# Performance work log

Measured on AMD Instinct MI355X. Metric: run time of the kernel, lower is better.

## Reference

```python
import jax, jax.numpy as jnp
import numpy as np

N, F_IN, H, OUT, E = 50000, 128, 128, 40, 800000


def setup_inputs() -> dict:
    key = jax.random.key(0)
    ks = jax.random.split(key, 20)
    s = 0.05
    return {
        "x": jax.random.normal(ks[0], (N, F_IN), jnp.float32),
        "edge_index": jax.random.randint(ks[1], (2, E), 0, N, jnp.int64),
        # GATConv (heads=1)
        "W_gat": jax.random.normal(ks[2], (F_IN, H), jnp.float32) * s,
        "att_src": jax.random.normal(ks[3], (H,), jnp.float32) * s,
        "att_dst": jax.random.normal(ks[4], (H,), jnp.float32) * s,
        "b_gat": jnp.zeros((H,), jnp.float32),
        # GCNConv
        "W_gcn": jax.random.normal(ks[5], (F_IN, H), jnp.float32) * s,
        "b_gcn": jnp.zeros((H,), jnp.float32),
        # SAGEConv (mean aggr): lin_l on neighbors (with bias), lin_r on root (no bias)
        "W_sage_l": jax.random.normal(ks[6], (F_IN, H), jnp.float32) * s,
        "b_sage_l": jnp.zeros((H,), jnp.float32),
        "W_sage_r": jax.random.normal(ks[7], (F_IN, H), jnp.float32) * s,
        # MLP head
        "W1": jax.random.normal(ks[8], (3 * H, 2 * H), jnp.float32) * s,
        "b1": jnp.zeros((2 * H,), jnp.float32),
        "W2": jax.random.normal(ks[9], (2 * H, H), jnp.float32) * s,
        "b2": jnp.zeros((H,), jnp.float32),
        "W3": jax.random.normal(ks[10], (H, OUT), jnp.float32) * s,
        "b3": jnp.zeros((OUT,), jnp.float32),
        # BatchNorm1d(3H)
        "gamma": jnp.ones((3 * H,), jnp.float32),
        "beta": jnp.zeros((3 * H,), jnp.float32),
    }


def _add_self_loops(edge_index, n):
    loop = jnp.arange(n, dtype=edge_index.dtype)
    src = jnp.concatenate([edge_index[0], loop])
    dst = jnp.concatenate([edge_index[1], loop])
    return src, dst


def _gat(x, src, dst, n, W, att_src, att_dst, bias):
    h = x @ W                                   # [N, H]
    a_s = h @ att_src                           # [N]
    a_d = h @ att_dst                           # [N]
    e = jax.nn.leaky_relu(a_s[src] + a_d[dst], 0.2)  # [E']
    m = jax.ops.segment_max(e, dst, num_segments=n)
    ex = jnp.exp(e - m[dst])
    denom = jax.ops.segment_sum(ex, dst, num_segments=n)
    alpha = ex / denom[dst]
    out = jax.ops.segment_sum(alpha[:, None] * h[src], dst, num_segments=n)
    return out + bias


def _gcn(x, src, dst, n, W, bias):
    h = x @ W
    deg = jax.ops.segment_sum(jnp.ones_like(dst, dtype=h.dtype), dst, num_segments=n)
    dinv = jnp.where(deg > 0, jax.lax.rsqrt(deg), 0.0)
    norm = dinv[src] * dinv[dst]                # [E']
    out = jax.ops.segment_sum(norm[:, None] * h[src], dst, num_segments=n)
    return out + bias


def _sage(x, src, dst, n, W_l, b_l, W_r):
    agg = jax.ops.segment_sum(x[src], dst, num_segments=n)
    cnt = jax.ops.segment_sum(jnp.ones_like(dst, dtype=x.dtype), dst, num_segments=n)
    mean = agg / jnp.maximum(cnt, 1.0)[:, None]
    return mean @ W_l + b_l + x @ W_r


def reference(x, edge_index, W_gat, att_src, att_dst, b_gat, W_gcn, b_gcn,
              W_sage_l, b_sage_l, W_sage_r, W1, b1, W2, b2, W3, b3, gamma, beta):
    n = x.shape[0]
    src, dst = edge_index[0], edge_index[1]          # SAGE: no self-loops
    src_sl, dst_sl = _add_self_loops(edge_index, n)  # GAT/GCN add self-loops

    x_gat = _gat(x, src_sl, dst_sl, n, W_gat, att_src, att_dst, b_gat)
    x_gcn = _gcn(x, src_sl, dst_sl, n, W_gcn, b_gcn)
    x_sage = _sage(x, src, dst, n, W_sage_l, b_sage_l, W_sage_r)

    h = jnp.concatenate([x_gat, x_gcn, x_sage], axis=1)  # [N, 3H]
    # BatchNorm1d (training-mode batch statistics; biased variance, eps=1e-5)
    mu = h.mean(axis=0)
    var = h.var(axis=0)
    h = (h - mu) * jax.lax.rsqrt(var + 1e-5) * gamma + beta
    # dropout is identity at inference
    h = jax.nn.relu(h) @ W1 + b1
    h = jax.nn.relu(h) @ W2 + b2
    h = jax.nn.relu(h) @ W3 + b3
    return h
```

## Files before the change

### kernel.cpp

```cpp
#include <hip/hip_runtime.h>
#include <cstdint>
#include <cstddef>

#define NN   50000
#define FIN  128
#define HD   128
#define EE   800000
#define C3   384
#define NOUT 40

#define NBLK ((NN + 127) / 128)

#define SPLIT_BLKS ((NN + 4) / 4)

#define NBUCK ((NN + 511) / 512)
#define BCAP  16384
#define BK_BLKS ((EE + 8191) / 8192)
#define SCAP  12288

#define RCAP      136
#define STORE_CAP 128
#define ZROW NN

#define LDSW 132

typedef __attribute__((ext_vector_type(8))) short s8v;
typedef __attribute__((ext_vector_type(4))) float f4v;
typedef __attribute__((ext_vector_type(8))) ushort u8v;

typedef const __attribute__((address_space(1))) unsigned int* guintp;
typedef __attribute__((address_space(3))) unsigned int* luintp;

static __device__ __forceinline__ void async_copy16(const void* g, void* l) {
    __builtin_amdgcn_global_load_lds((guintp)g, (luintp)l, 16, 0, 0);
}

static __device__ __forceinline__ float b2f(ushort u) {
    return __uint_as_float((unsigned)u << 16);
}
static __device__ __forceinline__ ushort f2b(float v) {
    unsigned u = __float_as_uint(v);
    unsigned r = u + 0x7fffu + ((u >> 16) & 1u);
    return (ushort)(r >> 16);
}

__global__ __launch_bounds__(256) void k_split_x_att(
    const float* __restrict__ x,
    const float* __restrict__ w_as, const float* __restrict__ w_ad,
    ushort* __restrict__ xb,
    float* __restrict__ a_s, float* __restrict__ a_d)
{
    int node = blockIdx.x * 4 + (threadIdx.x >> 6);
    if (node > NN) return;
    int lane = threadIdx.x & 63;
    size_t o = (size_t)node * 128 + lane * 2;
    if (node == NN) {
        ushort2 z; z.x = 0; z.y = 0;
        *(ushort2*)(xb + o) = z;
        return;
    }
    float2 v  = *(const float2*)(x + o);
    { ushort2 u; u.x = f2b(v.x); u.y = f2b(v.y); *(ushort2*)(xb + o) = u; }
    float2 w1 = *(const float2*)(w_as + lane * 2);
    float2 w2 = *(const float2*)(w_ad + lane * 2);
    float s1 = v.x * w1.x + v.y * w1.y;
    float s2 = v.x * w2.x + v.y * w2.y;
    #pragma unroll
    for (int off = 32; off; off >>= 1) {
        s1 += __shfl_down(s1, off);
        s2 += __shfl_down(s2, off);
    }
    if (lane == 0) { a_s[node] = s1; a_d[node] = s2; }
}

__global__ void k_splitw_all(
    const float* __restrict__ Wg, const float* __restrict__ Wc,
    const float* __restrict__ Wl, const float* __restrict__ Wr,
    const float* __restrict__ W1, const float* __restrict__ W2,
    const float* __restrict__ W3,
    const float* __restrict__ asv, const float* __restrict__ adv,
    float* __restrict__ w_as, float* __restrict__ w_ad,
    ushort* __restrict__ btg, ushort* __restrict__ btc,
    ushort* __restrict__ btsg,
    ushort* __restrict__ bt1, ushort* __restrict__ bt2,
    ushort* __restrict__ bt3)
{
    int ry = blockIdx.x;
    int t = threadIdx.x;
    if (ry == 816) {
        if (t < 128) {
            float s1 = 0.f, s2 = 0.f;
            for (int j = 0; j < 128; ++j) {
                float w = Wg[t * 128 + j];
                s1 += w * asv[j];
                s2 += w * adv[j];
            }
            w_as[t] = s1; w_ad[t] = s2;
        }
        return;
    }
    const float* W = nullptr; ushort* dh; int K, Nw, n;
    bool sage = false;
    if (ry < 128)      { n = ry;       K = 128; Nw = 128; W = Wg; dh = btg; }
    else if (ry < 256) { n = ry - 128; K = 128; Nw = 128; W = Wc; dh = btc; }
    else if (ry < 384) { n = ry - 256; K = 256; Nw = 128; sage = true; dh = btsg; }
    else if (ry < 640) { n = ry - 384; K = 384; Nw = 256; W = W1; dh = bt1; }
    else if (ry < 768) { n = ry - 640; K = 256; Nw = 128; W = W2; dh = bt2; }
    else               { n = ry - 768; K = 128; Nw = 40;  W = W3; dh = bt3; }
    for (int k = t; k < K; k += 256) {
        float v;
        if (sage) v = (k < 128) ? Wl[(size_t)k * 128 + n] : Wr[(size_t)(k - 128) * 128 + n];
        else      v = (n < Nw) ? W[(size_t)k * Nw + n] : 0.f;
        dh[(size_t)n * K + k] = f2b(v);
    }
}

template<int NT, int NCH, int AX, int BN>
__global__ __launch_bounds__(256, BN ? 4 : 5) void k_gemm2(
    const ushort* __restrict__ A, int K,
    const ushort* __restrict__ Bt,
    int M, int mode,
    const float* __restrict__ bias,
    float* __restrict__ Cf, int ldc,
    ushort* __restrict__ Ch, int ldch,
    int colmax,
    const float* __restrict__ bnscale, const float* __restrict__ bnshift)
{
    constexpr int COLS = NT * 16;
    constexpr int HOPU = 8 * COLS;
    constexpr int KTOT = NCH * 128;

    __shared__ __align__(16) ushort S[16384];
    __shared__ float bns[BN ? 768 : 4];
    ushort* Bs = S;
    ushort* As = S + 8192;

    const int lane = threadIdx.x & 63;
    const int wave = threadIdx.x >> 6;
    const int quad = lane >> 4;
    const int ln15 = lane & 15;
    const int brow = AX ? blockIdx.y : blockIdx.x;
    const int bcol = AX ? blockIdx.x : blockIdx.y;
    const int row0 = brow * 128 + wave * 32;
    const int col0 = bcol * COLS;
    const int Rbase = brow * 128;

    auto stageB = [&](int c, int h) {
        for (int u0 = wave * 64; u0 < HOPU; u0 += 256) {
            int u  = u0 + lane;
            int kq  = u / COLS;
            int col = u - kq * COLS;
            int kk  = c * 128 + h * 64 + kq * 8;
            const ushort* gp = Bt + (size_t)(col0 + col) * KTOT + kk;
            async_copy16(gp, (char*)Bs + (size_t)u0 * 16);
        }
    };
    auto stageA = [&](int c, int h) {
        #pragma unroll
        for (int i = 0; i < 4; ++i) {
            int u0 = (wave * 4 + i) * 64;
            int u  = u0 + lane;
            int row = u >> 3;
            int s   = u & 7;
            int sg  = s ^ (row & 7);
            int rr = Rbase + row; if (rr > M - 1) rr = M - 1;
            int kk = c * 128 + h * 64 + sg * 8;
            const ushort* gp = A + (size_t)rr * K + kk;
            async_copy16(gp, (char*)As + (size_t)u0 * 16);
        }
    };
    auto afrag = [&](int jj, int mt) -> s8v {
        int r = wave * 32 + mt * 16 + ln15;
        int sg = jj * 4 + quad;
        int unit = r * 8 + (sg ^ (r & 7));
        return *(const s8v*)(As + (size_t)unit * 8);
    };

    f4v acc[2][NT] = {};

    auto compute = [&](int jj, int kk0) {
        s8v a0 = afrag(jj, 0);
        s8v a1 = afrag(jj, 1);
        if constexpr (BN) {
            int cb0 = kk0 + (jj * 4 + quad) * 8;
            #pragma unroll
            for (int e = 0; e < 8; ++e) {
                float sc = bns[cb0 + e];
                float sh = bns[384 + cb0 + e];
                float v0 = b2f((ushort)a0[e]) * sc + sh;
                float v1 = b2f((ushort)a1[e]) * sc + sh;
                v0 = v0 > 0.f ? v0 : 0.f;
                v1 = v1 > 0.f ? v1 : 0.f;
                a0[e] = (short)f2b(v0);
                a1[e] = (short)f2b(v1);
            }
        }
        #pragma unroll
        for (int t = 0; t < NT; ++t) {
            int ub = (jj * 4 + quad) * COLS + t * 16 + ln15;
            s8v b = *(const s8v*)(Bs + (size_t)ub * 8);
            acc[0][t] = __builtin_amdgcn_mfma_f32_16x16x32_bf16(a0, b, acc[0][t], 0, 0, 0);
            acc[1][t] = __builtin_amdgcn_mfma_f32_16x16x32_bf16(a1, b, acc[1][t], 0, 0, 0);
        }
    };

    if constexpr (BN) {
        for (int j = threadIdx.x; j < 384; j += 256) {
            bns[j] = bnscale[j];
            bns[384 + j] = bnshift[j];
        }
    }
    stageB(0, 0); stageA(0, 0);
    __syncthreads();

    #pragma unroll
    for (int ph = 0; ph < NCH; ++ph) {
        #pragma unroll
        for (int h = 0; h < 2; ++h) {
            int kk0 = ph * 128 + h * 64;
            compute(0, kk0); compute(1, kk0);
            if (!(ph == NCH - 1 && h == 1)) {
                __syncthreads();
                int nc = ph, nh = h + 1;
                if (nh == 2) { nh = 0; ++nc; }
                stageB(nc, nh); stageA(nc, nh);
                __syncthreads();
            }
        }
    }

    if (NT == 8 && mode == 0) {
        __syncthreads();
        ushort* Lp = S + wave * 2176;
        #pragma unroll
        for (int mt = 0; mt < 2; ++mt) {
            #pragma unroll
            for (int t = 0; t < NT; ++t) {
                int cc = col0 + t * 16 + ln15;
                #pragma unroll
                for (int r = 0; r < 4; ++r) {
                    float v = acc[mt][t][r] + bias[cc];
                    v = v > 0.f ? v : 0.f;
                    Lp[(quad * 4 + r) * LDSW + t * 16 + ln15] = f2b(v);
                }
            }
            int cb = (lane & 31) * 4;
            #pragma unroll
            for (int it = 0; it < 8; ++it) {
                int row2 = it * 2 + (lane >> 5);
                int rr = row0 + mt * 16 + row2;
                uint2 v = *(uint2*)(Lp + row2 * LDSW + cb);
                if (rr < M)
                    *(uint2*)(Ch + (size_t)rr * ldch + col0 + cb) = v;
            }
        }
    } else {
        #pragma unroll
        for (int t = 0; t < NT; ++t) {
            int cc = col0 + t * 16 + ln15;
            #pragma unroll
            for (int mt = 0; mt < 2; ++mt) {
                #pragma unroll
                for (int r = 0; r < 4; ++r) {
                    int rr = row0 + mt * 16 + quad * 4 + r;
                    if (rr < M && cc < colmax)
                        Cf[(size_t)rr * ldc + cc] = acc[mt][t][r] + bias[cc];
                }
            }
        }
    }
}

__global__ __launch_bounds__(256, 3) void k_gemm_prod(
    const ushort* __restrict__ tgb, const ushort* __restrict__ tcb,
    const ushort* __restrict__ tsb, const ushort* __restrict__ xb,
    const ushort* __restrict__ btg, const ushort* __restrict__ btc,
    const ushort* __restrict__ btsg,
    const float* __restrict__ bg, const float* __restrict__ bc,
    const float* __restrict__ bsl,
    float* __restrict__ pS, float* __restrict__ pQ,
    ushort* __restrict__ hch)
{
    constexpr int COLS = 128;
    constexpr int HOPU = 8 * COLS;
    __shared__ __align__(16) ushort S[16384];
    ushort* Bs = S;
    ushort* As = S + 8192;
    float* red = (float*)(S + 14336);

    const int z = blockIdx.z;
    const ushort* A1 = (z == 0) ? tgb : (z == 1) ? tcb : tsb;
    const ushort* Bt = (z == 0) ? btg : (z == 1) ? btc : btsg;
    const float*  bias = (z == 0) ? bg : (z == 1) ? bc : bsl;
    const int nch = (z == 2) ? 2 : 1;
    const int ktot = nch * 128;

    const int lane = threadIdx.x & 63;
    const int wave = threadIdx.x >> 6;
    const int quad = lane >> 4;
    const int ln15 = lane & 15;
    const int row0 = blockIdx.x * 128 + wave * 32;
    const int Rbase = blockIdx.x * 128;

    auto stageB = [&](int c, int h) {
        for (int u0 = wave * 64; u0 < HOPU; u0 += 256) {
            int u  = u0 + lane;
            int kq  = u / COLS;
            int col = u - kq * COLS;
            int kk  = c * 128 + h * 64 + kq * 8;
            const ushort* gp = Bt + (size_t)col * ktot + kk;
            async_copy16(gp, (char*)Bs + (size_t)u0 * 16);
        }
    };
    auto stageA = [&](int c, int h) {
        #pragma unroll
        for (int i = 0; i < 4; ++i) {
            int u0 = (wave * 4 + i) * 64;
            int u  = u0 + lane;
            int row = u >> 3;
            int s   = u & 7;
            int sg  = s ^ (row & 7);
            int rr = Rbase + row; if (rr > NN - 1) rr = NN - 1;
            int kk = c * 128 + h * 64 + sg * 8;
            const ushort* gp = (kk < 128) ? (A1 + (size_t)rr * 128 + kk)
                                          : (xb + (size_t)rr * 128 + (kk - 128));
            async_copy16(gp, (char*)As + (size_t)u0 * 16);
        }
    };
    auto afrag = [&](int jj, int mt) -> s8v {
        int r = wave * 32 + mt * 16 + ln15;
        int sg = jj * 4 + quad;
        int unit = r * 8 + (sg ^ (r & 7));
        return *(const s8v*)(As + (size_t)unit * 8);
    };

    f4v acc[2][8] = {};

    auto compute = [&](int jj) {
        s8v a0 = afrag(jj, 0);
        s8v a1 = afrag(jj, 1);
        #pragma unroll
        for (int t = 0; t < 8; ++t) {
            int ub = (jj * 4 + quad) * COLS + t * 16 + ln15;
            s8v b = *(const s8v*)(Bs + (size_t)ub * 8);
            acc[0][t] = __builtin_amdgcn_mfma_f32_16x16x32_bf16(a0, b, acc[0][t], 0, 0, 0);
            acc[1][t] = __builtin_amdgcn_mfma_f32_16x16x32_bf16(a1, b, acc[1][t], 0, 0, 0);
        }
    };

    stageB(0, 0); stageA(0, 0);
    __syncthreads();

    for (int ph = 0; ph < nch; ++ph) {
        for (int h = 0; h < 2; ++h) {
            compute(0); compute(1);
            if (!(ph == nch - 1 && h == 1)) {
                __syncthreads();
                int nc = ph, nh = h + 1;
                if (nh == 2) { nh = 0; ++nc; }
                stageB(nc, nh); stageA(nc, nh);
                __syncthreads();
            }
        }
    }

    __syncthreads();
    if (threadIdx.x < 256) red[threadIdx.x] = 0.f;
    ushort* Lp = S + wave * 2176;
    float sp[8] = {}, qp[8] = {};
    #pragma unroll
    for (int mt = 0; mt < 2; ++mt) {
        #pragma unroll
        for (int t = 0; t < 8; ++t) {
            #pragma unroll
            for (int r = 0; r < 4; ++r) {
                int rr = row0 + mt * 16 + quad * 4 + r;
                float v = acc[mt][t][r] + bias[t * 16 + ln15];
                Lp[(quad * 4 + r) * LDSW + t * 16 + ln15] = f2b(v);
                if (rr < NN) { sp[t] += v; qp[t] += v * v; }
            }
        }
        int cb = (lane & 31) * 4;
        #pragma unroll
        for (int it = 0; it < 8; ++it) {
            int row2 = it * 2 + (lane >> 5);
            int rr = row0 + mt * 16 + row2;
            uint2 v = *(uint2*)(Lp + row2 * LDSW + cb);
            if (rr < NN)
                *(uint2*)(hch + (size_t)rr * C3 + z * 128 + cb) = v;
        }
    }
    __syncthreads();
    #pragma unroll
    for (int t = 0; t < 8; ++t) {
        float s = sp[t], q = qp[t];
        s += __shfl_xor(s, 16); s += __shfl_xor(s, 32);
        q += __shfl_xor(q, 16); q += __shfl_xor(q, 32);
        if (quad == 0) {
            atomicAdd(&red[t * 16 + ln15], s);
            atomicAdd(&red[128 + t * 16 + ln15], q);
        }
    }
    __syncthreads();
    if (threadIdx.x < 128) {
        size_t o = (size_t)blockIdx.x * C3 + z * 128 + threadIdx.x;
        pS[o] = red[threadIdx.x];
        pQ[o] = red[128 + threadIdx.x];
    }
}

__global__ __launch_bounds__(1024) void k_bucket(
    const int* __restrict__ e_src, const int* __restrict__ e_dst,
    int* __restrict__ bcnt, uint* __restrict__ ebuf)
{
    __shared__ uint sval[8192];
    __shared__ int scnt[NBUCK], sbase[NBUCK];
    int t = threadIdx.x;
    if (t < NBUCK) scnt[t] = 0;
    __syncthreads();
    int e0 = blockIdx.x * 8192;
    #pragma unroll
    for (int i = 0; i < 8; ++i) {
        int g = e0 + i * 1024 + t;
        uint val = 0xffffffffu;
        if (g < EE) {
            int d = e_dst[g];
            int s = e_src[g];
            int b = d >> 9;
            val = ((uint)b << 25) | ((uint)(d & 511) << 16) | (uint)s;
            atomicAdd(&scnt[b], 1);
        }
        sval[i * 1024 + t] = val;
    }
    __syncthreads();
    if (t < NBUCK) {
        sbase[t] = atomicAdd(&bcnt[t], scnt[t]);
        scnt[t] = 0;
    }
    __syncthreads();
    #pragma unroll
    for (int i = 0; i < 8; ++i) {
        uint val = sval[i * 1024 + t];
        if (val != 0xffffffffu) {
            int b = val >> 25;
            int lo = atomicAdd(&scnt[b], 1);
            ebuf[(size_t)b * BCAP + sbase[b] + lo] = val;
        }
    }
}

__global__ __launch_bounds__(1024) void k_degscan(
    const int* __restrict__ bcnt, const uint* __restrict__ ebuf,
    int* __restrict__ offs, float* __restrict__ dinv)
{
    __shared__ int hist[512];
    __shared__ int sh[256];
    __shared__ int btop;
    int b = blockIdx.x, t = threadIdx.x;
    int d0 = b * 512;
    if (t < 512) hist[t] = 0;
    __syncthreads();
    int nb = bcnt[b];
    const uint* eb = ebuf + (size_t)b * BCAP;
    for (int i = t; i < nb; i += 1024)
        atomicAdd(&hist[(eb[i] >> 16) & 511], 1);
    __syncthreads();
    if (t < 64) {
        int acc = 0;
        for (int i = t; i < b; i += 64) {
            int nd = NN - i * 512; if (nd > 512) nd = 512;
            acc += bcnt[i] + nd;
        }
        #pragma unroll
        for (int off = 32; off; off >>= 1) acc += __shfl_down(acc, off);
        if (t == 0) btop = acc;
    }
    int v0 = 0, v1 = 0;
    if (t < 256) {
        int i0g = d0 + t * 2;
        v0 = (i0g < NN) ? hist[t * 2] + 1 : 0;
        v1 = (i0g + 1 < NN) ? hist[t * 2 + 1] + 1 : 0;
        sh[t] = v0 + v1;
    }
    __syncthreads();
    for (int off = 1; off < 256; off <<= 1) {
        int u = 0;
        if (t < 256 && t >= off) u = sh[t - off];
        __syncthreads();
        if (t < 256) sh[t] += u;
        __syncthreads();
    }
    if (t < 256) {
        int pair = v0 + v1;
        int excl = sh[t] - pair + btop;
        int i0g = d0 + t * 2;
        if (i0g < NN)     { offs[i0g] = excl;          dinv[i0g] = rsqrtf((float)v0); }
        if (i0g + 1 < NN) { offs[i0g + 1] = excl + v0; dinv[i0g + 1] = rsqrtf((float)v1); }
        if (b == NBUCK - 1 && t == 255) offs[NN] = excl + pair;
    }
}

__global__ __launch_bounds__(1024) void k_csr_build(
    const int* __restrict__ bcnt, const uint* __restrict__ ebuf,
    const int* __restrict__ offs, ushort* __restrict__ esrc)
{
    __shared__ ushort sout[SCAP];
    __shared__ int cur[512];
    int b = blockIdx.x, t = threadIdx.x;
    int d0 = b * 512;
    int ndst = NN - d0; if (ndst > 512) ndst = 512;
    int obase = offs[d0];
    if (t < ndst) cur[t] = offs[d0 + t] - obase;
    __syncthreads();
    int nb = bcnt[b];
    const uint* eb = ebuf + (size_t)b * BCAP;
    for (int i = t; i < nb; i += 1024) {
        uint val = eb[i];
        int slot = atomicAdd(&cur[(val >> 16) & 511], 1);
        sout[slot] = (ushort)(val & 0xffffu);
    }
    if (t < ndst) {
        int slot = atomicAdd(&cur[t], 1);
        sout[slot] = (ushort)(d0 + t);
    }
    __syncthreads();
    int total = offs[d0 + ndst] - obase;
    for (int i = t; i < total; i += 1024)
        esrc[obase + i] = sout[i];
}

__global__ __launch_bounds__(256, 6) void k_gather(
    const ushort* __restrict__ esrc, const int* __restrict__ offs,
    const float* __restrict__ a_s, const float* __restrict__ a_d,
    const float* __restrict__ dinv,
    const ushort* __restrict__ xb,
    ushort* __restrict__ tgb, ushort* __restrict__ tcb,
    ushort* __restrict__ tsb)
{
    __shared__ uint2 recs[16][RCAP];
    int t = threadIdx.x;
    int qid = t >> 4;
    int ln = t & 15;
    int d = blockIdx.x * 16 + qid;
    if (d >= NN) return;
    uint2* rec = recs[qid];
    int beg = offs[d], end = offs[d + 1];
    int cnt = end - beg;
    float ad = a_d[d], dd = dinv[d];
    int stored = cnt < STORE_CAP ? cnt : STORE_CAP;

    float mloc = -3.0e38f;
    for (int b = 0; b < cnt; b += 16) {
        int j = b + ln;
        if (j < cnt) {
            int s = esrc[beg + j];
            float e = a_s[s] + ad;
            e = (e > 0.f) ? e : 0.2f * e;
            mloc = fmaxf(mloc, e);
            if (j < STORE_CAP) {
                uint2 r;
                r.x = __float_as_uint(e);
                r.y = (uint)s | ((uint)f2b(dinv[s] * dd) << 16);
                rec[j] = r;
            }
        }
    }
    float m = mloc;
    #pragma unroll
    for (int off = 1; off < 16; off <<= 1) m = fmaxf(m, __shfl_xor(m, off, 16));

    float denl = 0.f;
    for (int j = ln; j < stored; j += 16) {
        float ex = expf(__uint_as_float(rec[j].x) - m);
        denl += ex;
        rec[j].x = __float_as_uint(ex);
    }
    for (int idx = beg + STORE_CAP + ln; idx < end; idx += 16) {
        int s = esrc[idx];
        float e = a_s[s] + ad;
        e = (e > 0.f) ? e : 0.2f * e;
        denl += expf(e - m);
    }
    float den = denl;
    #pragma unroll
    for (int off = 1; off < 16; off <<= 1) den += __shfl_xor(den, off, 16);
    float rden = 1.f / den;

    for (int j = ln; j < stored; j += 16) {
        uint2 r = rec[j];
        uint2 q;
        q.x = (uint)f2b(__uint_as_float(r.x) * rden) | (r.y & 0xffff0000u);
        q.y = r.y & 0xffffu;
        rec[j] = q;
    }
    if (ln < 8) { uint2 q; q.x = 0u; q.y = (uint)ZROW; rec[stored + ln] = q; }

    float tg[8] = {}, tc[8] = {}, ts[8] = {};
    const ushort* xbs = xb + ln * 8;
    auto ldx = [&](uint srow) -> u8v {
        return *(const u8v*)(xbs + (size_t)srow * 128);
    };
    auto fmacc = [&](u8v x8, uint pw) {
        float wg = __uint_as_float(pw << 16);
        float wc = __uint_as_float(pw & 0xffff0000u);
        #pragma unroll
        for (int k = 0; k < 8; ++k) {
            float xv = b2f(x8[k]);
            tg[k] += wg * xv;
            tc[k] += wc * xv;
            ts[k] += xv;
        }
    };

    int P4 = (stored + 3) & ~3;
    uint pa0, pa1, pa2, pa3, pb0, pb1, pb2, pb3;
    u8v xa0, xa1, xa2, xa3, ya0, ya1, ya2, ya3;
    {
        uint2 r0 = rec[0], r1 = rec[1], r2 = rec[2], r3 = rec[3];
        pa0 = r0.x; xa0 = ldx(r0.y);
        pa1 = r1.x; xa1 = ldx(r1.y);
        pa2 = r2.x; xa2 = ldx(r2.y);
        pa3 = r3.x; xa3 = ldx(r3.y);
    }
    int j = 0;
    for (;;) {
        { uint2 r0 = rec[j+4], r1 = rec[j+5], r2 = rec[j+6], r3 = rec[j+7];
          pb0 = r0.x; ya0 = ldx(r0.y);
          pb1 = r1.x; ya1 = ldx(r1.y);
          pb2 = r2.x; ya2 = ldx(r2.y);
          pb3 = r3.x; ya3 = ldx(r3.y); }
        fmacc(xa0, pa0); fmacc(xa1, pa1); fmacc(xa2, pa2); fmacc(xa3, pa3);
        j += 4; if (j >= P4) break;
        { uint2 r0 = rec[j+4], r1 = rec[j+5], r2 = rec[j+6], r3 = rec[j+7];
          pa0 = r0.x; xa0 = ldx(r0.y);
          pa1 = r1.x; xa1 = ldx(r1.y);
          pa2 = r2.x; xa2 = ldx(r2.y);
          pa3 = r3.x; xa3 = ldx(r3.y); }
        fmacc(ya0, pb0); fmacc(ya1, pb1); fmacc(ya2, pb2); fmacc(ya3, pb3);
        j += 4; if (j >= P4) break;
    }

    for (int base = beg + STORE_CAP; base < end; base += 16) {
        int idx = base + ln;
        int s = ZROW; uint pw = 0;
        if (idx < end) {
            int ss = esrc[idx];
            float e = a_s[ss] + ad;
            e = (e > 0.f) ? e : 0.2f * e;
            pw = (uint)f2b(expf(e - m) * rden) | ((uint)f2b(dinv[ss] * dd) << 16);
            s = ss;
        }
        int cb = end - base; if (cb > 16) cb = 16;
        for (int jj = 0; jj < cb; ++jj) {
            int sa = __shfl(s, jj, 16);
            uint pa = (uint)__shfl((int)pw, jj, 16);
            fmacc(ldx((uint)sa), pa);
        }
    }

    u8v xd = *(const u8v*)(xb + (size_t)d * 128 + ln * 8);
    int cs = cnt - 1;
    float rc = 1.f / (float)(cs > 1 ? cs : 1);
    u8v og, oc, os;
    #pragma unroll
    for (int k = 0; k < 8; ++k) {
        og[k] = f2b(tg[k]);
        oc[k] = f2b(tc[k]);
        os[k] = f2b((ts[k] - b2f(xd[k])) * rc);
    }
    size_t row = (size_t)d * 128 + ln * 8;
    *(u8v*)(tgb + row) = og;
    *(u8v*)(tcb + row) = oc;
    *(u8v*)(tsb + row) = os;
}

__global__ void k_bn_final(const float* __restrict__ pS, const float* __restrict__ pQ,
                           const float* __restrict__ gamma, const float* __restrict__ beta,
                           float* __restrict__ scale, float* __restrict__ shift)
{
    int j = blockIdx.x * 64 + threadIdx.x;
    if (j >= C3) return;
    float s = 0.f, q = 0.f;
    for (int r = 0; r < NBLK; ++r) {
        s += pS[(size_t)r * C3 + j];
        q += pQ[(size_t)r * C3 + j];
    }
    const float rn = 1.f / (float)NN;
    float mu  = s * rn;
    float var = q * rn - mu * mu;
    float sc  = gamma[j] * rsqrtf(var + 1e-5f);
    scale[j] = sc;
    shift[j] = beta[j] - mu * sc;
}

extern "C" void kernel_launch(void* const* d_in, const int* in_sizes, int n_in,
                              void* d_out, int out_size, void* d_ws, size_t ws_size,
                              hipStream_t stream) {
    const float* x        = (const float*)d_in[0];
    const int*   ei       = (const int*)d_in[1];
    const float* W_gat    = (const float*)d_in[2];
    const float* att_src  = (const float*)d_in[3];
    const float* att_dst  = (const float*)d_in[4];
    const float* b_gat    = (const float*)d_in[5];
    const float* W_gcn    = (const float*)d_in[6];
    const float* b_gcn    = (const float*)d_in[7];
    const float* W_sage_l = (const float*)d_in[8];
    const float* b_sage_l = (const float*)d_in[9];
    const float* W_sage_r = (const float*)d_in[10];
    const float* W1       = (const float*)d_in[11];
    const float* b1       = (const float*)d_in[12];
    const float* W2       = (const float*)d_in[13];
    const float* b2       = (const float*)d_in[14];
    const float* W3       = (const float*)d_in[15];
    const float* b3       = (const float*)d_in[16];
    const float* gamma    = (const float*)d_in[17];
    const float* beta     = (const float*)d_in[18];

    const int* e_src = ei;
    const int* e_dst = ei + EE;

    char* base = (char*)d_ws;
    size_t o = 0;
    ushort* hch  = (ushort*)(base + o); o += (size_t)NN * C3 * 2;
    ushort* tgb  = (ushort*)(base + o); o += (size_t)NN * 128 * 2;
    ushort* tcb  = (ushort*)(base + o); o += (size_t)NN * 128 * 2;
    ushort* tsb  = (ushort*)(base + o); o += (size_t)NN * 128 * 2;
    ushort* xb   = (ushort*)(base + o); o += (size_t)(NN + 1) * 128 * 2;
    ushort* esrc = (ushort*)(base + o); o += ((size_t)(EE + NN) * 2 + 15) & ~15ull;
    int*    offs = (int*)(base + o);    o += (size_t)(NN + 16) * 4;
    float*  as_  = (float*)(base + o);  o += (size_t)NN * 4;
    float*  ad_  = (float*)(base + o);  o += (size_t)NN * 4;
    float*  dinv = (float*)(base + o);  o += (size_t)NN * 4;
    int*    bcnt = (int*)(base + o);    o += 128 * 4;
    float*  pS   = (float*)(base + o);  o += (size_t)NBLK * C3 * 4;
    float*  pQ   = (float*)(base + o);  o += (size_t)NBLK * C3 * 4;
    float*  scale= (float*)(base + o);  o += C3 * 4;
    float*  shift= (float*)(base + o);  o += C3 * 4;
    float*  w_as = (float*)(base + o);  o += 128 * 4;
    float*  w_ad = (float*)(base + o);  o += 128 * 4;
    ushort* btg  = (ushort*)(base + o); o += 128 * 128 * 2;
    ushort* btc  = (ushort*)(base + o); o += 128 * 128 * 2;
    ushort* btsg = (ushort*)(base + o); o += 128 * 256 * 2;
    ushort* bt1  = (ushort*)(base + o); o += 256 * 384 * 2;
    ushort* bt2  = (ushort*)(base + o); o += 128 * 256 * 2;
    ushort* bt3  = (ushort*)(base + o); o += 48 * 128 * 2;
    ushort* a1 = tgb;
    ushort* a2 = tsb;
    uint*   ebuf = (uint*)hch;

    hipMemsetAsync(bcnt, 0, 128 * 4, stream);

    k_splitw_all<<<817, 256, 0, stream>>>(W_gat, W_gcn, W_sage_l, W_sage_r, W1, W2, W3,
        att_src, att_dst, w_as, w_ad, btg, btc, btsg, bt1, bt2, bt3);
    k_split_x_att<<<SPLIT_BLKS, 256, 0, stream>>>(x, w_as, w_ad, xb, as_, ad_);

    k_bucket<<<BK_BLKS, 1024, 0, stream>>>(e_src, e_dst, bcnt, ebuf);
    k_degscan<<<NBUCK, 1024, 0, stream>>>(bcnt, ebuf, offs, dinv);
    k_csr_build<<<NBUCK, 1024, 0, stream>>>(bcnt, ebuf, offs, esrc);

    k_gather<<<(NN + 15) / 16, 256, 0, stream>>>(
        esrc, offs, as_, ad_, dinv, xb, tgb, tcb, tsb);

    k_gemm_prod<<<dim3(NBLK, 1, 3), 256, 0, stream>>>(
        tgb, tcb, tsb, xb, btg, btc, btsg,
        b_gat, b_gcn, b_sage_l, pS, pQ, hch);

    k_bn_final<<<6, 64, 0, stream>>>(pS, pQ, gamma, beta, scale, shift);

    k_gemm2<8, 3, 1, 1><<<dim3(2, NBLK), 256, 0, stream>>>(
        hch, 384, bt1, NN, 0, b1, nullptr, 0, a1, 256, 256, scale, shift);
    k_gemm2<8, 2, 0, 0><<<dim3(NBLK, 1), 256, 0, stream>>>(
        a1, 256, bt2, NN, 0, b2, nullptr, 0, a2, 128, 128, nullptr, nullptr);
    k_gemm2<3, 1, 0, 0><<<dim3(NBLK, 1), 256, 0, stream>>>(
        a2, 128, bt3, NN, 2, b3, (float*)d_out, NOUT, nullptr, 0, NOUT, nullptr, nullptr);
}
```

Baseline: 310.2 us.

## Fuse launch chain: merge bucket/weight prep, CSR build/x split, and final two GEMMs

Merges the weight-prep kernel into the edge bucketing launch and the x-to-bf16/attention-score kernel into a combined degree-scan plus CSR build kernel, which cuts the launch count. The last two MLP GEMMs are fused into one kernel that keeps the intermediate 128-wide activation in LDS and runs the 40-column output GEMM from there, so the a2 round trip through global memory goes away. The fused GEMM uses more LDS and has a lower occupancy bound. The k_bn_final block size changes and RCAP is reduced.

```diff
diff --git a/kernel.cpp b/kernel.cpp
--- a/kernel.cpp
+++ b/kernel.cpp
@@ -11,18 +11,18 @@
 
 #define NBLK ((NN + 127) / 128)
 
-#define SPLIT_BLKS ((NN + 4) / 4)
-
 #define NBUCK ((NN + 511) / 512)
 #define BCAP  16384
 #define BK_BLKS ((EE + 8191) / 8192)
 #define SCAP  12288
-
-#define RCAP      136
+#define SXB   ((NN + 16) / 16)
+
+#define RCAP      132
 #define STORE_CAP 128
 #define ZROW NN
 
 #define LDSW 132
+#define A2W  136
 
 typedef __attribute__((ext_vector_type(8))) short s8v;
 typedef __attribute__((ext_vector_type(4))) float f4v;
@@ -44,36 +44,9 @@
     return (ushort)(r >> 16);
 }
 
-__global__ __launch_bounds__(256) void k_split_x_att(
-    const float* __restrict__ x,
-    const float* __restrict__ w_as, const float* __restrict__ w_ad,
-    ushort* __restrict__ xb,
-    float* __restrict__ a_s, float* __restrict__ a_d)
-{
-    int node = blockIdx.x * 4 + (threadIdx.x >> 6);
-    if (node > NN) return;
-    int lane = threadIdx.x & 63;
-    size_t o = (size_t)node * 128 + lane * 2;
-    if (node == NN) {
-        ushort2 z; z.x = 0; z.y = 0;
-        *(ushort2*)(xb + o) = z;
-        return;
-    }
-    float2 v  = *(const float2*)(x + o);
-    { ushort2 u; u.x = f2b(v.x); u.y = f2b(v.y); *(ushort2*)(xb + o) = u; }
-    float2 w1 = *(const float2*)(w_as + lane * 2);
-    float2 w2 = *(const float2*)(w_ad + lane * 2);
-    float s1 = v.x * w1.x + v.y * w1.y;
-    float s2 = v.x * w2.x + v.y * w2.y;
-    #pragma unroll
-    for (int off = 32; off; off >>= 1) {
-        s1 += __shfl_down(s1, off);
-        s2 += __shfl_down(s2, off);
-    }
-    if (lane == 0) { a_s[node] = s1; a_d[node] = s2; }
-}
-
-__global__ void k_splitw_all(
+__global__ __launch_bounds__(1024) void k_bucketw(
+    const int* __restrict__ e_src, const int* __restrict__ e_dst,
+    int* __restrict__ bcnt, uint* __restrict__ ebuf,
     const float* __restrict__ Wg, const float* __restrict__ Wc,
     const float* __restrict__ Wl, const float* __restrict__ Wr,
     const float* __restrict__ W1, const float* __restrict__ W2,
@@ -85,337 +58,39 @@
     ushort* __restrict__ bt1, ushort* __restrict__ bt2,
     ushort* __restrict__ bt3)
 {
-    int ry = blockIdx.x;
     int t = threadIdx.x;
-    if (ry == 816) {
-        if (t < 128) {
-            float s1 = 0.f, s2 = 0.f;
-            for (int j = 0; j < 128; ++j) {
-                float w = Wg[t * 128 + j];
-                s1 += w * asv[j];
-                s2 += w * adv[j];
-            }
-            w_as[t] = s1; w_ad[t] = s2;
+    if (blockIdx.x >= BK_BLKS) {
+        int ry = blockIdx.x - BK_BLKS;
+        if (ry == 816) {
+            if (t < 128) {
+                float s1 = 0.f, s2 = 0.f;
+                for (int j = 0; j < 128; ++j) {
+                    float w = Wg[t * 128 + j];
+                    s1 += w * asv[j];
+                    s2 += w * adv[j];
+                }
+                w_as[t] = s1; w_ad[t] = s2;
+            }
+            return;
+        }
+        const float* W = nullptr; ushort* dh; int K, Nw, n;
+        bool sage = false;
+        if (ry < 128)      { n = ry;       K = 128; Nw = 128; W = Wg; dh = btg; }
+        else if (ry < 256) { n = ry - 128; K = 128; Nw = 128; W = Wc; dh = btc; }
+        else if (ry < 384) { n = ry - 256; K = 256; Nw = 128; sage = true; dh = btsg; }
+        else if (ry < 640) { n = ry - 384; K = 384; Nw = 256; W = W1; dh = bt1; }
+        else if (ry < 768) { n = ry - 640; K = 256; Nw = 128; W = W2; dh = bt2; }
+        else               { n = ry - 768; K = 128; Nw = 40;  W = W3; dh = bt3; }
+        for (int k = t; k < K; k += 1024) {
+            float v;
+            if (sage) v = (k < 128) ? Wl[(size_t)k * 128 + n] : Wr[(size_t)(k - 128) * 128 + n];
+            else      v = (n < Nw) ? W[(size_t)k * Nw + n] : 0.f;
+            dh[(size_t)n * K + k] = f2b(v);
         }
         return;
     }
-    const float* W = nullptr; ushort* dh; int K, Nw, n;
-    bool sage = false;
-    if (ry < 128)      { n = ry;       K = 128; Nw = 128; W = Wg; dh = btg; }
-    else if (ry < 256) { n = ry - 128; K = 128; Nw = 128; W = Wc; dh = btc; }
-    else if (ry < 384) { n = ry - 256; K = 256; Nw = 128; sage = true; dh = btsg; }
-    else if (ry < 640) { n = ry - 384; K = 384; Nw = 256; W = W1; dh = bt1; }
-    else if (ry < 768) { n = ry - 640; K = 256; Nw = 128; W = W2; dh = bt2; }
-    else               { n = ry - 768; K = 128; Nw = 40;  W = W3; dh = bt3; }
-    for (int k = t; k < K; k += 256) {
-        float v;
-        if (sage) v = (k < 128) ? Wl[(size_t)k * 128 + n] : Wr[(size_t)(k - 128) * 128 + n];
-        else      v = (n < Nw) ? W[(size_t)k * Nw + n] : 0.f;
-        dh[(size_t)n * K + k] = f2b(v);
-    }
-}
-
-template<int NT, int NCH, int AX, int BN>
-__global__ __launch_bounds__(256, BN ? 4 : 5) void k_gemm2(
-    const ushort* __restrict__ A, int K,
-    const ushort* __restrict__ Bt,
-    int M, int mode,
-    const float* __restrict__ bias,
-    float* __restrict__ Cf, int ldc,
-    ushort* __restrict__ Ch, int ldch,
-    int colmax,
-    const float* __restrict__ bnscale, const float* __restrict__ bnshift)
-{
-    constexpr int COLS = NT * 16;
-    constexpr int HOPU = 8 * COLS;
-    constexpr int KTOT = NCH * 128;
-
-    __shared__ __align__(16) ushort S[16384];
-    __shared__ float bns[BN ? 768 : 4];
-    ushort* Bs = S;
-    ushort* As = S + 8192;
-
-    const int lane = threadIdx.x & 63;
-    const int wave = threadIdx.x >> 6;
-    const int quad = lane >> 4;
-    const int ln15 = lane & 15;
-    const int brow = AX ? blockIdx.y : blockIdx.x;
-    const int bcol = AX ? blockIdx.x : blockIdx.y;
-    const int row0 = brow * 128 + wave * 32;
-    const int col0 = bcol * COLS;
-    const int Rbase = brow * 128;
-
-    auto stageB = [&](int c, int h) {
-        for (int u0 = wave * 64; u0 < HOPU; u0 += 256) {
-            int u  = u0 + lane;
-            int kq  = u / COLS;
-            int col = u - kq * COLS;
-            int kk  = c * 128 + h * 64 + kq * 8;
-            const ushort* gp = Bt + (size_t)(col0 + col) * KTOT + kk;
-            async_copy16(gp, (char*)Bs + (size_t)u0 * 16);
-        }
-    };
-    auto stageA = [&](int c, int h) {
-        #pragma unroll
-        for (int i = 0; i < 4; ++i) {
-            int u0 = (wave * 4 + i) * 64;
-            int u  = u0 + lane;
-            int row = u >> 3;
-            int s   = u & 7;
-            int sg  = s ^ (row & 7);
-            int rr = Rbase + row; if (rr > M - 1) rr = M - 1;
-            int kk = c * 128 + h * 64 + sg * 8;
-            const ushort* gp = A + (size_t)rr * K + kk;
-            async_copy16(gp, (char*)As + (size_t)u0 * 16);
-        }
-    };
-    auto afrag = [&](int jj, int mt) -> s8v {
-        int r = wave * 32 + mt * 16 + ln15;
-        int sg = jj * 4 + quad;
-        int unit = r * 8 + (sg ^ (r & 7));
-        return *(const s8v*)(As + (size_t)unit * 8);
-    };
-
-    f4v acc[2][NT] = {};
-
-    auto compute = [&](int jj, int kk0) {
-        s8v a0 = afrag(jj, 0);
-        s8v a1 = afrag(jj, 1);
-        if constexpr (BN) {
-            int cb0 = kk0 + (jj * 4 + quad) * 8;
-            #pragma unroll
-            for (int e = 0; e < 8; ++e) {
-                float sc = bns[cb0 + e];
-                float sh = bns[384 + cb0 + e];
-                float v0 = b2f((ushort)a0[e]) * sc + sh;
-                float v1 = b2f((ushort)a1[e]) * sc + sh;
-                v0 = v0 > 0.f ? v0 : 0.f;
-                v1 = v1 > 0.f ? v1 : 0.f;
-                a0[e] = (short)f2b(v0);
-                a1[e] = (short)f2b(v1);
-            }
-        }
-        #pragma unroll
-        for (int t = 0; t < NT; ++t) {
-            int ub = (jj * 4 + quad) * COLS + t * 16 + ln15;
-            s8v b = *(const s8v*)(Bs + (size_t)ub * 8);
-            acc[0][t] = __builtin_amdgcn_mfma_f32_16x16x32_bf16(a0, b, acc[0][t], 0, 0, 0);
-            acc[1][t] = __builtin_amdgcn_mfma_f32_16x16x32_bf16(a1, b, acc[1][t], 0, 0, 0);
-        }
-    };
-
-    if constexpr (BN) {
-        for (int j = threadIdx.x; j < 384; j += 256) {
-            bns[j] = bnscale[j];
-            bns[384 + j] = bnshift[j];
-        }
-    }
-    stageB(0, 0); stageA(0, 0);
-    __syncthreads();
-
-    #pragma unroll
-    for (int ph = 0; ph < NCH; ++ph) {
-        #pragma unroll
-        for (int h = 0; h < 2; ++h) {
-            int kk0 = ph * 128 + h * 64;
-            compute(0, kk0); compute(1, kk0);
-            if (!(ph == NCH - 1 && h == 1)) {
-                __syncthreads();
-                int nc = ph, nh = h + 1;
-                if (nh == 2) { nh = 0; ++nc; }
-                stageB(nc, nh); stageA(nc, nh);
-                __syncthreads();
-            }
-        }
-    }
-
-    if (NT == 8 && mode == 0) {
-        __syncthreads();
-        ushort* Lp = S + wave * 2176;
-        #pragma unroll
-        for (int mt = 0; mt < 2; ++mt) {
-            #pragma unroll
-            for (int t = 0; t < NT; ++t) {
-                int cc = col0 + t * 16 + ln15;
-                #pragma unroll
-                for (int r = 0; r < 4; ++r) {
-                    float v = acc[mt][t][r] + bias[cc];
-                    v = v > 0.f ? v : 0.f;
-                    Lp[(quad * 4 + r) * LDSW + t * 16 + ln15] = f2b(v);
-                }
-            }
-            int cb = (lane & 31) * 4;
-            #pragma unroll
-            for (int it = 0; it < 8; ++it) {
-                int row2 = it * 2 + (lane >> 5);
-                int rr = row0 + mt * 16 + row2;
-                uint2 v = *(uint2*)(Lp + row2 * LDSW + cb);
-                if (rr < M)
-                    *(uint2*)(Ch + (size_t)rr * ldch + col0 + cb) = v;
-            }
-        }
-    } else {
-        #pragma unroll
-        for (int t = 0; t < NT; ++t) {
-            int cc = col0 + t * 16 + ln15;
-            #pragma unroll
-            for (int mt = 0; mt < 2; ++mt) {
-                #pragma unroll
-                for (int r = 0; r < 4; ++r) {
-                    int rr = row0 + mt * 16 + quad * 4 + r;
-                    if (rr < M && cc < colmax)
-                        Cf[(size_t)rr * ldc + cc] = acc[mt][t][r] + bias[cc];
-                }
-            }
-        }
-    }
-}
-
-__global__ __launch_bounds__(256, 3) void k_gemm_prod(
-    const ushort* __restrict__ tgb, const ushort* __restrict__ tcb,
-    const ushort* __restrict__ tsb, const ushort* __restrict__ xb,
-    const ushort* __restrict__ btg, const ushort* __restrict__ btc,
-    const ushort* __restrict__ btsg,
-    const float* __restrict__ bg, const float* __restrict__ bc,
-    const float* __restrict__ bsl,
-    float* __restrict__ pS, float* __restrict__ pQ,
-    ushort* __restrict__ hch)
-{
-    constexpr int COLS = 128;
-    constexpr int HOPU = 8 * COLS;
-    __shared__ __align__(16) ushort S[16384];
-    ushort* Bs = S;
-    ushort* As = S + 8192;
-    float* red = (float*)(S + 14336);
-
-    const int z = blockIdx.z;
-    const ushort* A1 = (z == 0) ? tgb : (z == 1) ? tcb : tsb;
-    const ushort* Bt = (z == 0) ? btg : (z == 1) ? btc : btsg;
-    const float*  bias = (z == 0) ? bg : (z == 1) ? bc : bsl;
-    const int nch = (z == 2) ? 2 : 1;
-    const int ktot = nch * 128;
-
-    const int lane = threadIdx.x & 63;
-    const int wave = threadIdx.x >> 6;
-    const int quad = lane >> 4;
-    const int ln15 = lane & 15;
-    const int row0 = blockIdx.x * 128 + wave * 32;
-    const int Rbase = blockIdx.x * 128;
-
-    auto stageB = [&](int c, int h) {
-        for (int u0 = wave * 64; u0 < HOPU; u0 += 256) {
-            int u  = u0 + lane;
-            int kq  = u / COLS;
-            int col = u - kq * COLS;
-            int kk  = c * 128 + h * 64 + kq * 8;
-            const ushort* gp = Bt + (size_t)col * ktot + kk;
-            async_copy16(gp, (char*)Bs + (size_t)u0 * 16);
-        }
-    };
-    auto stageA = [&](int c, int h) {
-        #pragma unroll
-        for (int i = 0; i < 4; ++i) {
-            int u0 = (wave * 4 + i) * 64;
-            int u  = u0 + lane;
-            int row = u >> 3;
-            int s   = u & 7;
-            int sg  = s ^ (row & 7);
-            int rr = Rbase + row; if (rr > NN - 1) rr = NN - 1;
-            int kk = c * 128 + h * 64 + sg * 8;
-            const ushort* gp = (kk < 128) ? (A1 + (size_t)rr * 128 + kk)
-                                          : (xb + (size_t)rr * 128 + (kk - 128));
-            async_copy16(gp, (char*)As + (size_t)u0 * 16);
-        }
-    };
-    auto afrag = [&](int jj, int mt) -> s8v {
-        int r = wave * 32 + mt * 16 + ln15;
-        int sg = jj * 4 + quad;
-        int unit = r * 8 + (sg ^ (r & 7));
-        return *(const s8v*)(As + (size_t)unit * 8);
-    };
-
-    f4v acc[2][8] = {};
-
-    auto compute = [&](int jj) {
-        s8v a0 = afrag(jj, 0);
-        s8v a1 = afrag(jj, 1);
-        #pragma unroll
-        for (int t = 0; t < 8; ++t) {
-            int ub = (jj * 4 + quad) * COLS + t * 16 + ln15;
-            s8v b = *(const s8v*)(Bs + (size_t)ub * 8);
-            acc[0][t] = __builtin_amdgcn_mfma_f32_16x16x32_bf16(a0, b, acc[0][t], 0, 0, 0);
-            acc[1][t] = __builtin_amdgcn_mfma_f32_16x16x32_bf16(a1, b, acc[1][t], 0, 0, 0);
-        }
-    };
-
-    stageB(0, 0); stageA(0, 0);
-    __syncthreads();
-
-    for (int ph = 0; ph < nch; ++ph) {
-        for (int h = 0; h < 2; ++h) {
-            compute(0); compute(1);
-            if (!(ph == nch - 1 && h == 1)) {
-                __syncthreads();
-                int nc = ph, nh = h + 1;
-                if (nh == 2) { nh = 0; ++nc; }
-                stageB(nc, nh); stageA(nc, nh);
-                __syncthreads();
-            }
-        }
-    }
-
-    __syncthreads();
-    if (threadIdx.x < 256) red[threadIdx.x] = 0.f;
-    ushort* Lp = S + wave * 2176;
-    float sp[8] = {}, qp[8] = {};
-    #pragma unroll
-    for (int mt = 0; mt < 2; ++mt) {
-        #pragma unroll
-        for (int t = 0; t < 8; ++t) {
-            #pragma unroll
-            for (int r = 0; r < 4; ++r) {
-                int rr = row0 + mt * 16 + quad * 4 + r;
-                float v = acc[mt][t][r] + bias[t * 16 + ln15];
-                Lp[(quad * 4 + r) * LDSW + t * 16 + ln15] = f2b(v);
-                if (rr < NN) { sp[t] += v; qp[t] += v * v; }
-            }
-        }
-        int cb = (lane & 31) * 4;
-        #pragma unroll
-        for (int it = 0; it < 8; ++it) {
-            int row2 = it * 2 + (lane >> 5);
-            int rr = row0 + mt * 16 + row2;
-            uint2 v = *(uint2*)(Lp + row2 * LDSW + cb);
-            if (rr < NN)
-                *(uint2*)(hch + (size_t)rr * C3 + z * 128 + cb) = v;
-        }
-    }
-    __syncthreads();
-    #pragma unroll
-    for (int t = 0; t < 8; ++t) {
-        float s = sp[t], q = qp[t];
-        s += __shfl_xor(s, 16); s += __shfl_xor(s, 32);
-        q += __shfl_xor(q, 16); q += __shfl_xor(q, 32);
-        if (quad == 0) {
-            atomicAdd(&red[t * 16 + ln15], s);
-            atomicAdd(&red[128 + t * 16 + ln15], q);
-        }
-    }
-    __syncthreads();
-    if (threadIdx.x < 128) {
-        size_t o = (size_t)blockIdx.x * C3 + z * 128 + threadIdx.x;
-        pS[o] = red[threadIdx.x];
-        pQ[o] = red[128 + threadIdx.x];
-    }
-}
-
-__global__ __launch_bounds__(1024) void k_bucket(
-    const int* __restrict__ e_src, const int* __restrict__ e_dst,
-    int* __restrict__ bcnt, uint* __restrict__ ebuf)
-{
     __shared__ uint sval[8192];
     __shared__ int scnt[NBUCK], sbase[NBUCK];
-    int t = threadIdx.x;
     if (t < NBUCK) scnt[t] = 0;
     __syncthreads();
     int e0 = blockIdx.x * 8192;
@@ -449,15 +124,46 @@
     }
 }
 
-__global__ __launch_bounds__(1024) void k_degscan(
+__global__ __launch_bounds__(1024) void k_csrx(
     const int* __restrict__ bcnt, const uint* __restrict__ ebuf,
-    int* __restrict__ offs, float* __restrict__ dinv)
+    int* __restrict__ offs, float* __restrict__ dinv,
+    ushort* __restrict__ esrc,
+    const float* __restrict__ x,
+    const float* __restrict__ w_as, const float* __restrict__ w_ad,
+    ushort* __restrict__ xb, float* __restrict__ a_s, float* __restrict__ a_d)
 {
+    int t = threadIdx.x;
+    if (blockIdx.x >= NBUCK) {
+        int node = (blockIdx.x - NBUCK) * 16 + (t >> 6);
+        if (node > NN) return;
+        int lane = t & 63;
+        size_t o = (size_t)node * 128 + lane * 2;
+        if (node == NN) {
+            ushort2 z; z.x = 0; z.y = 0;
+            *(ushort2*)(xb + o) = z;
+            return;
+        }
+        float2 v  = *(const float2*)(x + o);
+        { ushort2 u; u.x = f2b(v.x); u.y = f2b(v.y); *(ushort2*)(xb + o) = u; }
+        float2 w1 = *(const float2*)(w_as + lane * 2);
+        float2 w2 = *(const float2*)(w_ad + lane * 2);
+        float s1 = v.x * w1.x + v.y * w1.y;
+        float s2 = v.x * w2.x + v.y * w2.y;
+        #pragma unroll
+        for (int off = 32; off; off >>= 1) {
+            s1 += __shfl_down(s1, off);
+            s2 += __shfl_down(s2, off);
+        }
+        if (lane == 0) { a_s[node] = s1; a_d[node] = s2; }
+        return;
+    }
+    __shared__ ushort sout[SCAP];
     __shared__ int hist[512];
     __shared__ int sh[256];
-    __shared__ int btop;
-    int b = blockIdx.x, t = threadIdx.x;
+    __shared__ int btop_s;
+    int b = blockIdx.x;
     int d0 = b * 512;
+    int ndst = NN - d0; if (ndst > 512) ndst = 512;
     if (t < 512) hist[t] = 0;
     __syncthreads();
     int nb = bcnt[b];
@@ -473,7 +179,7 @@
         }
         #pragma unroll
         for (int off = 32; off; off >>= 1) acc += __shfl_down(acc, off);
-        if (t == 0) btop = acc;
+        if (t == 0) btop_s = acc;
     }
     int v0 = 0, v1 = 0;
     if (t < 256) {
@@ -492,44 +198,37 @@
     }
     if (t < 256) {
         int pair = v0 + v1;
-        int excl = sh[t] - pair + btop;
+        int lex = sh[t] - pair;
+        int excl = lex + btop_s;
         int i0g = d0 + t * 2;
-        if (i0g < NN)     { offs[i0g] = excl;          dinv[i0g] = rsqrtf((float)v0); }
-        if (i0g + 1 < NN) { offs[i0g + 1] = excl + v0; dinv[i0g + 1] = rsqrtf((float)v1); }
+        if (i0g < NN) {
+            offs[i0g] = excl; dinv[i0g] = rsqrtf((float)v0);
+            hist[t * 2] = lex;
+        }
+        if (i0g + 1 < NN) {
+            offs[i0g + 1] = excl + v0; dinv[i0g + 1] = rsqrtf((float)v1);
+            hist[t * 2 + 1] = lex + v0;
+        }
         if (b == NBUCK - 1 && t == 255) offs[NN] = excl + pair;
     }
-}
-
-__global__ __launch_bounds__(1024) void k_csr_build(
-    const int* __restrict__ bcnt, const uint* __restrict__ ebuf,
-    const int* __restrict__ offs, ushort* __restrict__ esrc)
-{
-    __shared__ ushort sout[SCAP];
-    __shared__ int cur[512];
-    int b = blockIdx.x, t = threadIdx.x;
-    int d0 = b * 512;
-    int ndst = NN - d0; if (ndst > 512) ndst = 512;
-    int obase = offs[d0];
-    if (t < ndst) cur[t] = offs[d0 + t] - obase;
-    __syncthreads();
-    int nb = bcnt[b];
-    const uint* eb = ebuf + (size_t)b * BCAP;
+    __syncthreads();
     for (int i = t; i < nb; i += 1024) {
         uint val = eb[i];
-        int slot = atomicAdd(&cur[(val >> 16) & 511], 1);
+        int slot = atomicAdd(&hist[(val >> 16) & 511], 1);
         sout[slot] = (ushort)(val & 0xffffu);
     }
     if (t < ndst) {
-        int slot = atomicAdd(&cur[t], 1);
+        int slot = atomicAdd(&hist[t], 1);
         sout[slot] = (ushort)(d0 + t);
     }
     __syncthreads();
-    int total = offs[d0 + ndst] - obase;
+    int total = nb + ndst;
+    int obase = btop_s;
     for (int i = t; i < total; i += 1024)
         esrc[obase + i] = sout[i];
 }
 
-__global__ __launch_bounds__(256, 6) void k_gather(
+__global__ __launch_bounds__(256) void k_gather(
     const ushort* __restrict__ esrc, const int* __restrict__ offs,
     const float* __restrict__ a_s, const float* __restrict__ a_d,
     const float* __restrict__ dinv,
@@ -593,7 +292,7 @@
         q.y = r.y & 0xffffu;
         rec[j] = q;
     }
-    if (ln < 8) { uint2 q; q.x = 0u; q.y = (uint)ZROW; rec[stored + ln] = q; }
+    if (ln < 2) { uint2 q; q.x = 0u; q.y = (uint)ZROW; rec[stored + ln] = q; }
 
     float tg[8] = {}, tc[8] = {}, ts[8] = {};
     const ushort* xbs = xb + ln * 8;
@@ -612,32 +311,17 @@
         }
     };
 
-    int P4 = (stored + 3) & ~3;
-    uint pa0, pa1, pa2, pa3, pb0, pb1, pb2, pb3;
-    u8v xa0, xa1, xa2, xa3, ya0, ya1, ya2, ya3;
-    {
-        uint2 r0 = rec[0], r1 = rec[1], r2 = rec[2], r3 = rec[3];
-        pa0 = r0.x; xa0 = ldx(r0.y);
-        pa1 = r1.x; xa1 = ldx(r1.y);
-        pa2 = r2.x; xa2 = ldx(r2.y);
-        pa3 = r3.x; xa3 = ldx(r3.y);
-    }
+    int Pcnt = (stored + 1) & ~1;
+    uint2 rA = rec[0]; u8v xA = ldx(rA.y);
+    uint2 rB; u8v xB;
     int j = 0;
     for (;;) {
-        { uint2 r0 = rec[j+4], r1 = rec[j+5], r2 = rec[j+6], r3 = rec[j+7];
-          pb0 = r0.x; ya0 = ldx(r0.y);
-          pb1 = r1.x; ya1 = ldx(r1.y);
-          pb2 = r2.x; ya2 = ldx(r2.y);
-          pb3 = r3.x; ya3 = ldx(r3.y); }
-        fmacc(xa0, pa0); fmacc(xa1, pa1); fmacc(xa2, pa2); fmacc(xa3, pa3);
-        j += 4; if (j >= P4) break;
-        { uint2 r0 = rec[j+4], r1 = rec[j+5], r2 = rec[j+6], r3 = rec[j+7];
-          pa0 = r0.x; xa0 = ldx(r0.y);
-          pa1 = r1.x; xa1 = ldx(r1.y);
-          pa2 = r2.x; xa2 = ldx(r2.y);
-          pa3 = r3.x; xa3 = ldx(r3.y); }
-        fmacc(ya0, pb0); fmacc(ya1, pb1); fmacc(ya2, pb2); fmacc(ya3, pb3);
-        j += 4; if (j >= P4) break;
+        rB = rec[j + 1]; xB = ldx(rB.y);
+        fmacc(xA, rA.x);
+        if (++j >= Pcnt) break;
+        rA = rec[j + 1]; xA = ldx(rA.y);
+        fmacc(xB, rB.x);
+        if (++j >= Pcnt) break;
     }
 
     for (int base = beg + STORE_CAP; base < end; base += 16) {
@@ -674,23 +358,463 @@
     *(u8v*)(tsb + row) = os;
 }
 
+__global__ __launch_bounds__(256, 3) void k_gemm_prod(
+    const ushort* __restrict__ tgb, const ushort* __restrict__ tcb,
+    const ushort* __restrict__ tsb, const ushort* __restrict__ xb,
+    const ushort* __restrict__ btg, const ushort* __restrict__ btc,
+    const ushort* __restrict__ btsg,
+    const float* __restrict__ bg, const float* __restrict__ bc,
+    const float* __restrict__ bsl,
+    float* __restrict__ pS, float* __restrict__ pQ,
+    ushort* __restrict__ hch)
+{
+    constexpr int COLS = 128;
+    constexpr int HOPU = 8 * COLS;
+    __shared__ __align__(16) ushort S[16384];
+    ushort* Bs = S;
+    ushort* As = S + 8192;
+    float* red = (float*)(S + 14336);
+
+    const int z = blockIdx.z;
+    const ushort* A1 = (z == 0) ? tgb : (z == 1) ? tcb : tsb;
+    const ushort* Bt = (z == 0) ? btg : (z == 1) ? btc : btsg;
+    const float*  bias = (z == 0) ? bg : (z == 1) ? bc : bsl;
+    const int nch = (z == 2) ? 2 : 1;
+    const int ktot = nch * 128;
+
+    const int lane = threadIdx.x & 63;
+    const int wave = threadIdx.x >> 6;
+    const int quad = lane >> 4;
+    const int ln15 = lane & 15;
+    const int row0 = blockIdx.x * 128 + wave * 32;
+    const int Rbase = blockIdx.x * 128;
+
+    auto stageB = [&](int c, int h) {
+        for (int u0 = wave * 64; u0 < HOPU; u0 += 256) {
+            int u  = u0 + lane;
+            int kq  = u / COLS;
+            int col = u - kq * COLS;
+            int kk  = c * 128 + h * 64 + kq * 8;
+            const ushort* gp = Bt + (size_t)col * ktot + kk;
+            async_copy16(gp, (char*)Bs + (size_t)u0 * 16);
+        }
+    };
+    auto stageA = [&](int c, int h) {
+        #pragma unroll
+        for (int i = 0; i < 4; ++i) {
+            int u0 = (wave * 4 + i) * 64;
+            int u  = u0 + lane;
+            int row = u >> 3;
+            int s   = u & 7;
+            int sg  = s ^ (row & 7);
+            int rr = Rbase + row; if (rr > NN - 1) rr = NN - 1;
+            int kk = c * 128 + h * 64 + sg * 8;
+            const ushort* gp = (kk < 128) ? (A1 + (size_t)rr * 128 + kk)
+                                          : (xb + (size_t)rr * 128 + (kk - 128));
+            async_copy16(gp, (char*)As + (size_t)u0 * 16);
+        }
+    };
+    auto afrag = [&](int jj, int mt) -> s8v {
+        int r = wave * 32 + mt * 16 + ln15;
+        int sg = jj * 4 + quad;
+        int unit = r * 8 + (sg ^ (r & 7));
+        return *(const s8v*)(As + (size_t)unit * 8);
+    };
+
+    f4v acc[2][8] = {};
+
+    auto compute = [&](int jj) {
+        s8v a0 = afrag(jj, 0);
+        s8v a1 = afrag(jj, 1);
+        #pragma unroll
+        for (int t = 0; t < 8; ++t) {
+            int ub = (jj * 4 + quad) * COLS + t * 16 + ln15;
+            s8v b = *(const s8v*)(Bs + (size_t)ub * 8);
+            acc[0][t] = __builtin_amdgcn_mfma_f32_16x16x32_bf16(a0, b, acc[0][t], 0, 0, 0);
+            acc[1][t] = __builtin_amdgcn_mfma_f32_16x16x32_bf16(a1, b, acc[1][t], 0, 0, 0);
+        }
+    };
+
+    stageB(0, 0); stageA(0, 0);
+    __syncthreads();
+
+    for (int ph = 0; ph < nch; ++ph) {
+        for (int h = 0; h < 2; ++h) {
+            compute(0); compute(1);
+            if (!(ph == nch - 1 && h == 1)) {
+                __syncthreads();
+                int nc = ph, nh = h + 1;
+                if (nh == 2) { nh = 0; ++nc; }
+                stageB(nc, nh); stageA(nc, nh);
+                __syncthreads();
+            }
+        }
+    }
+
+    __syncthreads();
+    if (threadIdx.x < 256) red[threadIdx.x] = 0.f;
+    ushort* Lp = S + wave * 2176;
+    float sp[8] = {}, qp[8] = {};
+    #pragma unroll
+    for (int mt = 0; mt < 2; ++mt) {
+        #pragma unroll
+        for (int t = 0; t < 8; ++t) {
+            #pragma unroll
+            for (int r = 0; r < 4; ++r) {
+                int rr = row0 + mt * 16 + quad * 4 + r;
+                float v = acc[mt][t][r] + bias[t * 16 + ln15];
+                Lp[(quad * 4 + r) * LDSW + t * 16 + ln15] = f2b(v);
+                if (rr < NN) { sp[t] += v; qp[t] += v * v; }
+            }
+        }
+        int cb = (lane & 31) * 4;
+        #pragma unroll
+        for (int it = 0; it < 8; ++it) {
+            int row2 = it * 2 + (lane >> 5);
+            int rr = row0 + mt * 16 + row2;
+            uint2 v = *(uint2*)(Lp + row2 * LDSW + cb);
+            if (rr < NN)
+                *(uint2*)(hch + (size_t)rr * C3 + z * 128 + cb) = v;
+        }
+    }
+    __syncthreads();
+    #pragma unroll
+    for (int t = 0; t < 8; ++t) {
+        float s = sp[t], q = qp[t];
+        s += __shfl_xor(s, 16); s += __shfl_xor(s, 32);
+        q += __shfl_xor(q, 16); q += __shfl_xor(q, 32);
+        if (quad == 0) {
+            atomicAdd(&red[t * 16 + ln15], s);
+            atomicAdd(&red[128 + t * 16 + ln15], q);
+        }
+    }
+    __syncthreads();
+    if (threadIdx.x < 128) {
+        size_t o = (size_t)blockIdx.x * C3 + z * 128 + threadIdx.x;
+        pS[o] = red[threadIdx.x];
+        pQ[o] = red[128 + threadIdx.x];
+    }
+}
+
 __global__ void k_bn_final(const float* __restrict__ pS, const float* __restrict__ pQ,
                            const float* __restrict__ gamma, const float* __restrict__ beta,
                            float* __restrict__ scale, float* __restrict__ shift)
 {
-    int j = blockIdx.x * 64 + threadIdx.x;
+    int t = threadIdx.x;
+    int j = blockIdx.x * 64 + (t >> 2);
+    int part = t & 3;
     if (j >= C3) return;
     float s = 0.f, q = 0.f;
-    for (int r = 0; r < NBLK; ++r) {
+    for (int r = part; r < NBLK; r += 4) {
         s += pS[(size_t)r * C3 + j];
         q += pQ[(size_t)r * C3 + j];
     }
-    const float rn = 1.f / (float)NN;
-    float mu  = s * rn;
-    float var = q * rn - mu * mu;
-    float sc  = gamma[j] * rsqrtf(var + 1e-5f);
-    scale[j] = sc;
-    shift[j] = beta[j] - mu * sc;
+    s += __shfl_down(s, 2); s += __shfl_down(s, 1);
+    q += __shfl_down(q, 2); q += __shfl_down(q, 1);
+    if (part == 0) {
+        const float rn = 1.f / (float)NN;
+        float mu  = s * rn;
+        float var = q * rn - mu * mu;
+        float sc  = gamma[j] * rsqrtf(var + 1e-5f);
+        scale[j] = sc;
+        shift[j] = beta[j] - mu * sc;
+    }
+}
+
+template<int NT, int NCH, int AX, int BN>
+__global__ __launch_bounds__(256, BN ? 4 : 5) void k_gemm2(
+    const ushort* __restrict__ A, int K,
+    const ushort* __restrict__ Bt,
+    int M, int mode,
+    const float* __restrict__ bias,
+    float* __restrict__ Cf, int ldc,
+    ushort* __restrict__ Ch, int ldch,
+    int colmax,
+    const float* __restrict__ bnscale, const float* __restrict__ bnshift)
+{
+    constexpr int COLS = NT * 16;
+    constexpr int HOPU = 8 * COLS;
+    constexpr int KTOT = NCH * 128;
+
+    __shared__ __align__(16) ushort S[16384];
+    __shared__ float bns[BN ? 768 : 4];
+    ushort* Bs = S;
+    ushort* As = S + 8192;
+
+    const int lane = threadIdx.x & 63;
+    const int wave = threadIdx.x >> 6;
+    const int quad = lane >> 4;
+    const int ln15 = lane & 15;
+    const int brow = AX ? blockIdx.y : blockIdx.x;
+    const int bcol = AX ? blockIdx.x : blockIdx.y;
+    const int row0 = brow * 128 + wave * 32;
+    const int col0 = bcol * COLS;
+    const int Rbase = brow * 128;
+
+    auto stageB = [&](int c, int h) {
+        for (int u0 = wave * 64; u0 < HOPU; u0 += 256) {
+            int u  = u0 + lane;
+            int kq  = u / COLS;
+            int col = u - kq * COLS;
+            int kk  = c * 128 + h * 64 + kq * 8;
+            const ushort* gp = Bt + (size_t)(col0 + col) * KTOT + kk;
+            async_copy16(gp, (char*)Bs + (size_t)u0 * 16);
+        }
+    };
+    auto stageA = [&](int c, int h) {
+        #pragma unroll
+        for (int i = 0; i < 4; ++i) {
+            int u0 = (wave * 4 + i) * 64;
+            int u  = u0 + lane;
+            int row = u >> 3;
+            int s   = u & 7;
+            int sg  = s ^ (row & 7);
+            int rr = Rbase + row; if (rr > M - 1) rr = M - 1;
+            int kk = c * 128 + h * 64 + sg * 8;
+            const ushort* gp = A + (size_t)rr * K + kk;
+            async_copy16(gp, (char*)As + (size_t)u0 * 16);
+        }
+    };
+    auto afrag = [&](int jj, int mt) -> s8v {
+        int r = wave * 32 + mt * 16 + ln15;
+        int sg = jj * 4 + quad;
+        int unit = r * 8 + (sg ^ (r & 7));
+        return *(const s8v*)(As + (size_t)unit * 8);
+    };
+
+    f4v acc[2][NT] = {};
+
+    auto compute = [&](int jj, int kk0) {
+        s8v a0 = afrag(jj, 0);
+        s8v a1 = afrag(jj, 1);
+        if constexpr (BN) {
+            int cb0 = kk0 + (jj * 4 + quad) * 8;
+            #pragma unroll
+            for (int e = 0; e < 8; ++e) {
+                float sc = bns[cb0 + e];
+                float sh = bns[384 + cb0 + e];
+                float v0 = b2f((ushort)a0[e]) * sc + sh;
+                float v1 = b2f((ushort)a1[e]) * sc + sh;
+                v0 = v0 > 0.f ? v0 : 0.f;
+                v1 = v1 > 0.f ? v1 : 0.f;
+                a0[e] = (short)f2b(v0);
+                a1[e] = (short)f2b(v1);
+            }
+        }
+        #pragma unroll
+        for (int t = 0; t < NT; ++t) {
+            int ub = (jj * 4 + quad) * COLS + t * 16 + ln15;
+            s8v b = *(const s8v*)(Bs + (size_t)ub * 8);
+            acc[0][t] = __builtin_amdgcn_mfma_f32_16x16x32_bf16(a0, b, acc[0][t], 0, 0, 0);
+            acc[1][t] = __builtin_amdgcn_mfma_f32_16x16x32_bf16(a1, b, acc[1][t], 0, 0, 0);
+        }
+    };
+
+    if constexpr (BN) {
+        for (int j = threadIdx.x; j < 384; j += 256) {
+            bns[j] = bnscale[j];
+            bns[384 + j] = bnshift[j];
+        }
+    }
+    stageB(0, 0); stageA(0, 0);
+    __syncthreads();
+
+    #pragma unroll
+    for (int ph = 0; ph < NCH; ++ph) {
+        #pragma unroll
+        for (int h = 0; h < 2; ++h) {
+            int kk0 = ph * 128 + h * 64;
+            compute(0, kk0); compute(1, kk0);
+            if (!(ph == NCH - 1 && h == 1)) {
+                __syncthreads();
+                int nc = ph, nh = h + 1;
+                if (nh == 2) { nh = 0; ++nc; }
+                stageB(nc, nh); stageA(nc, nh);
+                __syncthreads();
+            }
+        }
+    }
+
+    if (NT == 8 && mode == 0) {
+        __syncthreads();
+        ushort* Lp = S + wave * 2176;
+        #pragma unroll
+        for (int mt = 0; mt < 2; ++mt) {
+            #pragma unroll
+            for (int t = 0; t < NT; ++t) {
+                int cc = col0 + t * 16 + ln15;
+                #pragma unroll
+                for (int r = 0; r < 4; ++r) {
+                    float v = acc[mt][t][r] + bias[cc];
+                    v = v > 0.f ? v : 0.f;
+                    Lp[(quad * 4 + r) * LDSW + t * 16 + ln15] = f2b(v);
+                }
+            }
+            int cb = (lane & 31) * 4;
+            #pragma unroll
+            for (int it = 0; it < 8; ++it) {
+                int row2 = it * 2 + (lane >> 5);
+                int rr = row0 + mt * 16 + row2;
+                uint2 v = *(uint2*)(Lp + row2 * LDSW + cb);
+                if (rr < M)
+                    *(uint2*)(Ch + (size_t)rr * ldch + col0 + cb) = v;
+            }
+        }
+    } else {
+        #pragma unroll
+        for (int t = 0; t < NT; ++t) {
+            int cc = col0 + t * 16 + ln15;
+            #pragma unroll
+            for (int mt = 0; mt < 2; ++mt) {
+                #pragma unroll
+                for (int r = 0; r < 4; ++r) {
+                    int rr = row0 + mt * 16 + quad * 4 + r;
+                    if (rr < M && cc < colmax)
+                        Cf[(size_t)rr * ldc + cc] = acc[mt][t][r] + bias[cc];
+                }
+            }
+        }
+    }
+}
+
+__global__ __launch_bounds__(256, 2) void k_gemm23(
+    const ushort* __restrict__ A,
+    const ushort* __restrict__ Bt2, const ushort* __restrict__ Bt3,
+    const float* __restrict__ b2v, const float* __restrict__ b3v,
+    float* __restrict__ out)
+{
+    constexpr int COLS = 128;
+    constexpr int HOPU = 1024;
+    constexpr int KTOT = 256;
+    __shared__ __align__(16) ushort S[16384];
+    __shared__ __align__(16) ushort A2[128 * A2W];
+    ushort* Bs = S;
+    ushort* As = S + 8192;
+
+    const int lane = threadIdx.x & 63;
+    const int wave = threadIdx.x >> 6;
+    const int quad = lane >> 4;
+    const int ln15 = lane & 15;
+    const int Rbase = blockIdx.x * 128;
+    const int row0 = Rbase + wave * 32;
+
+    auto stageB = [&](int c, int h) {
+        for (int u0 = wave * 64; u0 < HOPU; u0 += 256) {
+            int u  = u0 + lane;
+            int kq  = u / COLS;
+            int col = u - kq * COLS;
+            int kk  = c * 128 + h * 64 + kq * 8;
+            async_copy16(Bt2 + (size_t)col * KTOT + kk, (char*)Bs + (size_t)u0 * 16);
+        }
+    };
+    auto stageA = [&](int c, int h) {
+        #pragma unroll
+        for (int i = 0; i < 4; ++i) {
+            int u0 = (wave * 4 + i) * 64;
+            int u  = u0 + lane;
+            int row = u >> 3;
+            int s   = u & 7;
+            int sg  = s ^ (row & 7);
+            int rr = Rbase + row; if (rr > NN - 1) rr = NN - 1;
+            int kk = c * 128 + h * 64 + sg * 8;
+            async_copy16(A + (size_t)rr * KTOT + kk, (char*)As + (size_t)u0 * 16);
+        }
+    };
+    auto afrag = [&](int jj, int mt) -> s8v {
+        int r = wave * 32 + mt * 16 + ln15;
+        int sg = jj * 4 + quad;
+        int unit = r * 8 + (sg ^ (r & 7));
+        return *(const s8v*)(As + (size_t)unit * 8);
+    };
+
+    f4v acc[2][8] = {};
+    auto compute = [&](int jj) {
+        s8v a0 = afrag(jj, 0);
+        s8v a1 = afrag(jj, 1);
+        #pragma unroll
+        for (int t = 0; t < 8; ++t) {
+            int ub = (jj * 4 + quad) * COLS + t * 16 + ln15;
+            s8v b = *(const s8v*)(Bs + (size_t)ub * 8);
+            acc[0][t] = __builtin_amdgcn_mfma_f32_16x16x32_bf16(a0, b, acc[0][t], 0, 0, 0);
+            acc[1][t] = __builtin_amdgcn_mfma_f32_16x16x32_bf16(a1, b, acc[1][t], 0, 0, 0);
+        }
+    };
+
+    stageB(0, 0); stageA(0, 0);
+    __syncthreads();
+    #pragma unroll
+    for (int ph = 0; ph < 2; ++ph) {
+        #pragma unroll
+        for (int h = 0; h < 2; ++h) {
+            compute(0); compute(1);
+            if (!(ph == 1 && h == 1)) {
+                __syncthreads();
+                int nc = ph, nh = h + 1;
+                if (nh == 2) { nh = 0; ++nc; }
+                stageB(nc, nh); stageA(nc, nh);
+                __syncthreads();
+            }
+        }
+    }
+
+    __syncthreads();
+    for (int u0 = wave * 64; u0 < 768; u0 += 256) {
+        int u = u0 + lane;
+        int h = u / 384;
+        int rem = u - h * 384;
+        int kq = rem / 48;
+        int col = rem - kq * 48;
+        int kk = h * 64 + kq * 8;
+        async_copy16(Bt3 + (size_t)col * 128 + kk, (char*)S + (size_t)u0 * 16);
+    }
+    #pragma unroll
+    for (int mt = 0; mt < 2; ++mt) {
+        #pragma unroll
+        for (int t = 0; t < 8; ++t) {
+            int cc = t * 16 + ln15;
+            float bb = b2v[cc];
+            #pragma unroll
+            for (int r = 0; r < 4; ++r) {
+                int rl = wave * 32 + mt * 16 + quad * 4 + r;
+                float v = acc[mt][t][r] + bb;
+                v = v > 0.f ? v : 0.f;
+                A2[(size_t)rl * A2W + cc] = f2b(v);
+            }
+        }
+    }
+    __syncthreads();
+
+    f4v acc3[2][3] = {};
+    #pragma unroll
+    for (int h = 0; h < 2; ++h) {
+        #pragma unroll
+        for (int jj = 0; jj < 2; ++jj) {
+            int sg = jj * 4 + quad;
+            int ko = h * 64 + sg * 8;
+            s8v a0 = *(const s8v*)(A2 + (size_t)(wave * 32 + ln15) * A2W + ko);
+            s8v a1 = *(const s8v*)(A2 + (size_t)(wave * 32 + 16 + ln15) * A2W + ko);
+            #pragma unroll
+            for (int t = 0; t < 3; ++t) {
+                int ub = h * 384 + sg * 48 + t * 16 + ln15;
+                s8v b = *(const s8v*)(S + (size_t)ub * 8);
+                acc3[0][t] = __builtin_amdgcn_mfma_f32_16x16x32_bf16(a0, b, acc3[0][t], 0, 0, 0);
+                acc3[1][t] = __builtin_amdgcn_mfma_f32_16x16x32_bf16(a1, b, acc3[1][t], 0, 0, 0);
+            }
+        }
+    }
+    #pragma unroll
+    for (int t = 0; t < 3; ++t) {
+        int cc = t * 16 + ln15;
+        #pragma unroll
+        for (int mt = 0; mt < 2; ++mt) {
+            #pragma unroll
+            for (int r = 0; r < 4; ++r) {
+                int rr = row0 + mt * 16 + quad * 4 + r;
+                if (rr < NN && cc < NOUT)
+                    out[(size_t)rr * NOUT + cc] = acc3[mt][t][r] + b3v[cc];
+            }
+        }
+    }
 }
 
 extern "C" void kernel_launch(void* const* d_in, const int* in_sizes, int n_in,
@@ -745,18 +869,18 @@
     ushort* bt2  = (ushort*)(base + o); o += 128 * 256 * 2;
     ushort* bt3  = (ushort*)(base + o); o += 48 * 128 * 2;
     ushort* a1 = tgb;
-    ushort* a2 = tsb;
     uint*   ebuf = (uint*)hch;
 
     hipMemsetAsync(bcnt, 0, 128 * 4, stream);
 
-    k_splitw_all<<<817, 256, 0, stream>>>(W_gat, W_gcn, W_sage_l, W_sage_r, W1, W2, W3,
+    k_bucketw<<<BK_BLKS + 817, 1024, 0, stream>>>(
+        e_src, e_dst, bcnt, ebuf,
+        W_gat, W_gcn, W_sage_l, W_sage_r, W1, W2, W3,
         att_src, att_dst, w_as, w_ad, btg, btc, btsg, bt1, bt2, bt3);
-    k_split_x_att<<<SPLIT_BLKS, 256, 0, stream>>>(x, w_as, w_ad, xb, as_, ad_);
-
-    k_bucket<<<BK_BLKS, 1024, 0, stream>>>(e_src, e_dst, bcnt, ebuf);
-    k_degscan<<<NBUCK, 1024, 0, stream>>>(bcnt, ebuf, offs, dinv);
-    k_csr_build<<<NBUCK, 1024, 0, stream>>>(bcnt, ebuf, offs, esrc);
+
+    k_csrx<<<NBUCK + SXB, 1024, 0, stream>>>(
+        bcnt, ebuf, offs, dinv, esrc,
+        x, w_as, w_ad, xb, as_, ad_);
 
     k_gather<<<(NN + 15) / 16, 256, 0, stream>>>(
         esrc, offs, as_, ad_, dinv, xb, tgb, tcb, tsb);
@@ -765,12 +889,10 @@
         tgb, tcb, tsb, xb, btg, btc, btsg,
         b_gat, b_gcn, b_sage_l, pS, pQ, hch);
 
-    k_bn_final<<<6, 64, 0, stream>>>(pS, pQ, gamma, beta, scale, shift);
+    k_bn_final<<<6, 256, 0, stream>>>(pS, pQ, gamma, beta, scale, shift);
 
     k_gemm2<8, 3, 1, 1><<<dim3(2, NBLK), 256, 0, stream>>>(
         hch, 384, bt1, NN, 0, b1, nullptr, 0, a1, 256, 256, scale, shift);
-    k_gemm2<8, 2, 0, 0><<<dim3(NBLK, 1), 256, 0, stream>>>(
-        a1, 256, bt2, NN, 0, b2, nullptr, 0, a2, 128, 128, nullptr, nullptr);
-    k_gemm2<3, 1, 0, 0><<<dim3(NBLK, 1), 256, 0, stream>>>(
-        a2, 128, bt3, NN, 2, b3, (float*)d_out, NOUT, nullptr, 0, NOUT, nullptr, nullptr);
-}
+
+    k_gemm23<<<NBLK, 256, 0, stream>>>(a1, bt2, bt3, b2, b3, (float*)d_out);
+}
```

Measured after the change: 271.4 us (median of 2 runs). -12.5%, faster.
